# Optimization experiments

Measured on AMD Instinct MI355X. Metric: run time of the kernel, lower is better.

Reference implementation:

```python
import jax, jax.numpy as jnp
import numpy as np

K = 3          # kernel size
PAD = (K - 1) // 2


def setup_inputs() -> dict:
    key = jax.random.key(0)
    k1, k2, k3 = jax.random.split(key, 3)
    x = jax.random.normal(k1, (32, 512, 56, 56), jnp.float32)
    # offset predictor conv1d weight: (out=K, in=1, kw=K), no bias
    w_offset = jax.random.normal(k2, (K, 1, K), jnp.float32) * 0.1
    # deformable conv1d(1,1,K) weight (K,) and scalar bias
    w_deform = jax.random.normal(k3, (K,), jnp.float32) * 0.5
    b_deform = jnp.zeros((), jnp.float32)
    return {"x": x, "w_offset": w_offset, "w_deform": w_deform, "b_deform": b_deform}


def _dca_forward(x, w_offset, w_deform, b_deform):
    b, c, h, w = x.shape
    # AdaptiveAvgPool2d(1) -> channel descriptor (b, c)
    y = x.mean(axis=(2, 3))
    # conv_offset_local: Conv1d(1, K, kernel=K, pad=PAD) on (b, 1, c) -> (b, K, c)
    offset = jax.lax.conv_general_dilated(
        y[:, None, :], w_offset, window_strides=(1,),
        padding=[(PAD, PAD)], dimension_numbers=("NCH", "OIH", "NCH"))
    # deformable sampling positions: p + k - PAD + offset[b,k,p], shape (b, K, c)
    pos = (jnp.arange(c, dtype=x.dtype)[None, None, :]
           + jnp.arange(K, dtype=x.dtype)[None, :, None]
           - PAD + offset)
    p0 = jnp.floor(pos)
    frac = pos - p0                     # (b, K, c), differentiable wrt offset
    p0i = p0.astype(jnp.int32)

    def sample(idx):
        # linear gather from y with zero padding outside [0, c)
        valid = (idx >= 0) & (idx < c)
        idxc = jnp.clip(idx, 0, c - 1)
        v = jax.vmap(lambda yb, ib: yb[ib])(y, idxc)   # (b, K, c)
        return jnp.where(valid, v, jnp.zeros((), x.dtype))

    v = sample(p0i) * (1.0 - frac) + sample(p0i + 1) * frac
    out = jnp.einsum("k,bkc->bc", w_deform, v) + b_deform   # (b, c)
    attn = jax.nn.sigmoid(out)[:, :, None, None]
    return attn * x


def reference(x, w_offset, w_deform, b_deform):
    return _dca_forward(x, w_offset, w_deform, b_deform)
```

## Files before the change

kernel.cpp:

```cpp
#include <hip/hip_runtime.h>
#include <hip/hip_bf16.h>
#include <math.h>

#define B 32
#define C 512
#define HW 3136
#define HW4 784
#define KS 3
#define PADK 1

__global__ __launch_bounds__(256) void mean_kernel(const float* __restrict__ x,
                                                   float* __restrict__ y) {
    const int plane = blockIdx.x;
    const float4* xp = (const float4*)(x + (size_t)plane * HW);
    float s = 0.f;
    for (int i = threadIdx.x; i < HW4; i += 256) {
        float4 v = xp[i];
        s += (v.x + v.y) + (v.z + v.w);
    }
    #pragma unroll
    for (int o = 32; o > 0; o >>= 1) s += __shfl_down(s, o, 64);
    __shared__ float red[4];
    const int wave = threadIdx.x >> 6;
    const int lane = threadIdx.x & 63;
    if (lane == 0) red[wave] = s;
    __syncthreads();
    if (threadIdx.x == 0) {
        float t = (red[0] + red[1]) + (red[2] + red[3]);
        y[plane] = t * (1.0f / (float)HW);
    }
}

__global__ __launch_bounds__(512) void attn_kernel(const float* __restrict__ y,
                                                   const float* __restrict__ w_offset,
                                                   const float* __restrict__ w_deform,
                                                   const float* __restrict__ b_deform,
                                                   float* __restrict__ attn) {
    const int b = blockIdx.x;
    const int p = threadIdx.x;
    __shared__ float ys[C];
    ys[p] = y[b * C + p];
    __syncthreads();

    const float ym1 = (p >= 1)     ? ys[p - 1] : 0.f;
    const float y0  = ys[p];
    const float yp1 = (p < C - 1)  ? ys[p + 1] : 0.f;

    float acc = b_deform[0];
    #pragma unroll
    for (int k = 0; k < KS; ++k) {
        const float off = w_offset[k * KS + 0] * ym1
                        + w_offset[k * KS + 1] * y0
                        + w_offset[k * KS + 2] * yp1;
        const float pos  = (float)(p + k - PADK) + off;
        const float p0f  = floorf(pos);
        const float frac = pos - p0f;
        const int   i0   = (int)p0f;
        const int   i1   = i0 + 1;
        const float v0 = (i0 >= 0 && i0 < C) ? ys[i0] : 0.f;
        const float v1 = (i1 >= 0 && i1 < C) ? ys[i1] : 0.f;
        acc += w_deform[k] * (v0 * (1.f - frac) + v1 * frac);
    }
    attn[b * C + p] = 1.f / (1.f + expf(-acc));
}

__global__ __launch_bounds__(256) void scale_kernel(const float* __restrict__ x,
                                                    const float* __restrict__ attn,
                                                    float* __restrict__ out) {
    const int plane = blockIdx.x;
    const float a = attn[plane];
    const float4* xp = (const float4*)(x + (size_t)plane * HW);
    float4*       op = (float4*)(out + (size_t)plane * HW);
    for (int i = threadIdx.x; i < HW4; i += 256) {
        float4 v = xp[i];
        v.x *= a; v.y *= a; v.z *= a; v.w *= a;
        op[i] = v;
    }
}

extern "C" void kernel_launch(void* const* d_in, const int* in_sizes, int n_in,
                              void* d_out, int out_size, void* d_ws, size_t ws_size,
                              hipStream_t stream) {
    const float* x        = (const float*)d_in[0];
    const float* w_offset = (const float*)d_in[1];
    const float* w_deform = (const float*)d_in[2];
    const float* b_deform = (const float*)d_in[3];
    float* out  = (float*)d_out;

    float* y    = (float*)d_ws;
    float* attn = y + B * C;

    mean_kernel<<<B * C, 256, 0, stream>>>(x, y);
    attn_kernel<<<B, C, 0, stream>>>(y, w_offset, w_deform, b_deform, attn);
    scale_kernel<<<B * C, 256, 0, stream>>>(x, attn, out);
}
```

Before: 381.2 us.

## Fuse attention computation into scale kernel and use nontemporal output stores

Removes the separate attention kernel launch. Each scale block's first thread now computes its channel's sigmoid attention directly from the pooled means and shares it through LDS. Output writes use nontemporal stores so the streamed result does not pollute the cache. This drops one launch and the attn round trip, but every block now runs a serial scalar prologue with dependent global loads before it can start streaming.

```diff
diff --git a/kernel.cpp b/kernel.cpp
--- a/kernel.cpp
+++ b/kernel.cpp
@@ -9,13 +9,15 @@
 #define KS 3
 #define PADK 1
 
+typedef float fvec4 __attribute__((ext_vector_type(4)));
+
 __global__ __launch_bounds__(256) void mean_kernel(const float* __restrict__ x,
                                                    float* __restrict__ y) {
     const int plane = blockIdx.x;
-    const float4* xp = (const float4*)(x + (size_t)plane * HW);
+    const fvec4* xp = (const fvec4*)(x + (size_t)plane * HW);
     float s = 0.f;
     for (int i = threadIdx.x; i < HW4; i += 256) {
-        float4 v = xp[i];
+        fvec4 v = xp[i];
         s += (v.x + v.y) + (v.z + v.w);
     }
     #pragma unroll
@@ -31,50 +33,50 @@
     }
 }
 
-__global__ __launch_bounds__(512) void attn_kernel(const float* __restrict__ y,
-                                                   const float* __restrict__ w_offset,
-                                                   const float* __restrict__ w_deform,
-                                                   const float* __restrict__ b_deform,
-                                                   float* __restrict__ attn) {
-    const int b = blockIdx.x;
-    const int p = threadIdx.x;
-    __shared__ float ys[C];
-    ys[p] = y[b * C + p];
+__global__ __launch_bounds__(256) void scale_attn_kernel(
+        const float* __restrict__ x,
+        const float* __restrict__ y,
+        const float* __restrict__ w_offset,
+        const float* __restrict__ w_deform,
+        const float* __restrict__ b_deform,
+        float* __restrict__ out) {
+    const int plane = blockIdx.x;
+    const int b = plane >> 9;
+    const int p = plane & (C - 1);
+    __shared__ float a_sh;
+
+    if (threadIdx.x == 0) {
+        const float* yb = y + b * C;
+        const float ym1 = (p >= 1)     ? yb[p - 1] : 0.f;
+        const float y0  = yb[p];
+        const float yp1 = (p < C - 1)  ? yb[p + 1] : 0.f;
+
+        float acc = b_deform[0];
+        #pragma unroll
+        for (int k = 0; k < KS; ++k) {
+            const float off = w_offset[k * KS + 0] * ym1
+                            + w_offset[k * KS + 1] * y0
+                            + w_offset[k * KS + 2] * yp1;
+            const float pos  = (float)(p + k - PADK) + off;
+            const float p0f  = floorf(pos);
+            const float frac = pos - p0f;
+            const int   i0   = (int)p0f;
+            const int   i1   = i0 + 1;
+            const float v0 = (i0 >= 0 && i0 < C) ? yb[i0] : 0.f;
+            const float v1 = (i1 >= 0 && i1 < C) ? yb[i1] : 0.f;
+            acc += w_deform[k] * (v0 * (1.f - frac) + v1 * frac);
+        }
+        a_sh = 1.f / (1.f + expf(-acc));
+    }
     __syncthreads();
+    const float a = a_sh;
 
-    const float ym1 = (p >= 1)     ? ys[p - 1] : 0.f;
-    const float y0  = ys[p];
-    const float yp1 = (p < C - 1)  ? ys[p + 1] : 0.f;
-
-    float acc = b_deform[0];
-    #pragma unroll
-    for (int k = 0; k < KS; ++k) {
-        const float off = w_offset[k * KS + 0] * ym1
-                        + w_offset[k * KS + 1] * y0
-                        + w_offset[k * KS + 2] * yp1;
-        const float pos  = (float)(p + k - PADK) + off;
-        const float p0f  = floorf(pos);
-        const float frac = pos - p0f;
-        const int   i0   = (int)p0f;
-        const int   i1   = i0 + 1;
-        const float v0 = (i0 >= 0 && i0 < C) ? ys[i0] : 0.f;
-        const float v1 = (i1 >= 0 && i1 < C) ? ys[i1] : 0.f;
-        acc += w_deform[k] * (v0 * (1.f - frac) + v1 * frac);
-    }
-    attn[b * C + p] = 1.f / (1.f + expf(-acc));
-}
-
-__global__ __launch_bounds__(256) void scale_kernel(const float* __restrict__ x,
-                                                    const float* __restrict__ attn,
-                                                    float* __restrict__ out) {
-    const int plane = blockIdx.x;
-    const float a = attn[plane];
-    const float4* xp = (const float4*)(x + (size_t)plane * HW);
-    float4*       op = (float4*)(out + (size_t)plane * HW);
+    const fvec4* xp = (const fvec4*)(x + (size_t)plane * HW);
+    fvec4*       op = (fvec4*)(out + (size_t)plane * HW);
     for (int i = threadIdx.x; i < HW4; i += 256) {
-        float4 v = xp[i];
-        v.x *= a; v.y *= a; v.z *= a; v.w *= a;
-        op[i] = v;
+        fvec4 v = xp[i];
+        v *= a;
+        __builtin_nontemporal_store(v, &op[i]);
     }
 }
 
@@ -87,10 +89,9 @@
     const float* b_deform = (const float*)d_in[3];
     float* out  = (float*)d_out;
 
-    float* y    = (float*)d_ws;
-    float* attn = y + B * C;
+    float* y = (float*)d_ws;
 
     mean_kernel<<<B * C, 256, 0, stream>>>(x, y);
-    attn_kernel<<<B, C, 0, stream>>>(y, w_offset, w_deform, b_deform, attn);
-    scale_kernel<<<B * C, 256, 0, stream>>>(x, attn, out);
+    scale_attn_kernel<<<B * C, 256, 0, stream>>>(x, y, w_offset, w_deform,
+                                                 b_deform, out);
 }
```

Result: faster. 370.3 us (-2.9%).
